# Kernel tuning notes

Hardware: AMD Instinct MI355X
Metric: run time of the kernel (lower is better)

## Reference

```python
import jax, jax.numpy as jnp
import numpy as np

NUM_ITERS = 3

def squash(t, axis):
    # scale = |t|^2/(1+|t|^2); out = scale * t / |t|
    sn = jnp.sum(t * t, axis=axis, keepdims=True)
    return (sn / (1.0 + sn)) * t / jnp.sqrt(sn)


def setup_inputs() -> dict:
    key = jax.random.key(0)
    k1, k2, k3, k4 = jax.random.split(key, 4)
    B = 128
    inputs = jax.random.normal(k1, (B, 256, 20, 20), dtype=jnp.float32)
    conv_w = jax.random.normal(k2, (8, 32, 256, 9, 9), dtype=jnp.float32) * 0.05
    conv_b = jax.random.normal(k3, (8, 32), dtype=jnp.float32) * 0.05
    route_weights = jax.random.normal(k4, (10, 1152, 8, 16), dtype=jnp.float32)
    return {"inputs": inputs, "conv_w": conv_w, "conv_b": conv_b,
            "route_weights": route_weights}


def reference(inputs, conv_w, conv_b, route_weights):
    B = inputs.shape[0]
    K, O, Cin, kh, kw = conv_w.shape          # 8 capsules, 32 out-chans each
    # --- primary capsules: 8 parallel convs fused into one grouped-output conv ---
    w = conv_w.reshape(K * O, Cin, kh, kw)
    out = jax.lax.conv_general_dilated(
        inputs, w, window_strides=(2, 2), padding='VALID',
        dimension_numbers=('NCHW', 'OIHW', 'NCHW'))  # [B, K*O, 6, 6]
    out = out + conv_b.reshape(K * O)[None, :, None, None]
    H = out.shape[-1]
    x = out.reshape(B, K, O * H * H).transpose(0, 2, 1)  # [B, 1152, 8]
    x = squash(x, axis=2)
    # --- routing layer ---
    # prediction_vectors: x[None,:,:,None,:] @ W[:,None,:,:,:] -> [10,B,1152,1,16]
    pred = jnp.einsum('bri,crio->cbro', x, route_weights)[:, :, :, None, :]
    logits = jnp.zeros_like(pred)
    v = None
    for i in range(NUM_ITERS):
        # routing_softmax(dim=2): softmax over the routes axis (faithful to source)
        c = jax.nn.softmax(logits, axis=2)
        s = jnp.sum(c * pred, axis=2, keepdims=True)  # [10,B,1,1,16]
        v = squash(s, axis=1)                          # squash default dim=1 (batch) -- faithful
        if i != NUM_ITERS - 1:
            logits = logits + jnp.sum(pred * v, axis=-1, keepdims=True)
    # [10,B,1,1,16] -> squeeze -> [10,B,16] -> permute(1,0,2) -> [B,10,16]
    return jnp.squeeze(v).transpose(1, 0, 2)
```

## Files before the change

kernel.cpp:

```cpp
#include <hip/hip_runtime.h>
#include <math.h>

typedef _Float16 f16;
typedef _Float16 f16x8 __attribute__((ext_vector_type(8)));
typedef float f32x4 __attribute__((ext_vector_type(4)));
typedef float f32x8 __attribute__((ext_vector_type(8)));

#define AS1 __attribute__((address_space(1)))
#define AS3 __attribute__((address_space(3)))

__device__ __forceinline__ void gld_lds16(const f16* g, f16* l) {
#if defined(__has_builtin) && __has_builtin(__builtin_amdgcn_global_load_lds)
    __builtin_amdgcn_global_load_lds((const AS1 void*)g, (AS3 void*)l, 16, 0, 0);
#else
    *(uint4*)l = *(const uint4*)g;
#endif
}

__global__ __launch_bounds__(256) void transpose_input(
    const float* __restrict__ inp, f16* __restrict__ out)
{
    const int b = blockIdx.x, c0 = blockIdx.y * 32, p0 = blockIdx.z * 32;
    const int tx = threadIdx.x, ty = threadIdx.y;
    __shared__ float t[32][33];
#pragma unroll
    for (int j = 0; j < 4; ++j) {
        int c = ty + j * 8, p = p0 + tx;
        if (p < 400) t[c][tx] = inp[((size_t)b * 256 + c0 + c) * 400 + p];
    }
    __syncthreads();
#pragma unroll
    for (int j = 0; j < 4; ++j) {
        int p = p0 + ty + j * 8;
        if (p < 400) out[((size_t)b * 400 + p) * 256 + c0 + tx] = (f16)t[tx][ty + j * 8];
    }
}

__global__ __launch_bounds__(256) void permute_w(
    const float* __restrict__ cw, f16* __restrict__ w_t)
{
    const int n = blockIdx.x, t = threadIdx.x;
    __shared__ f16 buf[81 * 258];
    const float* src = cw + (size_t)n * 20736;
    for (int i = t; i < 20736; i += 256) {
        int cin = i / 81, p = i - cin * 81;
        buf[p * 258 + cin] = (f16)src[i];
    }
    __syncthreads();
    f16* dst = w_t + (size_t)n * 20736;
    for (int j = t; j < 20736; j += 256) {
        int p = j >> 8, cin = j & 255;
        dst[j] = buf[p * 258 + cin];
    }
}

#define SPLITK 9
#define CITER 72
__global__ __launch_bounds__(256) void conv_mfma(
    const f16* __restrict__ in_t,
    const f16* __restrict__ w_t,
    float* __restrict__ part)
{
    __shared__ f16 As[2][128 * 32];
    __shared__ f16 Bs[2][128 * 32];
    const int tid = threadIdx.x;
    const int lane = tid & 63, wave = tid >> 6;
    const int wm = wave >> 1, wn = wave & 1;
    const int m0 = blockIdx.x * 128, n0 = blockIdx.y * 128;
    const int kz = blockIdx.z;

    int srcA[2], srcB[2];
#pragma unroll
    for (int i = 0; i < 2; ++i) {
        int pairp = i * 32 + (tid >> 3);
        int chunk8 = (tid & 7) ^ (pairp & 7);
        int e = chunk8 >> 2, q4 = chunk8 & 3;
        int m = m0 + pairp * 2 + e;
        int b = m / 36, hw = m - b * 36;
        int ho = hw / 6, wo = hw - ho * 6;
        srcA[i] = ((b * 20 + 2 * ho) * 20 + 2 * wo) * 256 + q4 * 8;
        int n = n0 + pairp * 2 + e;
        srcB[i] = n * 20736 + q4 * 8;
    }

    f32x4 acc[4][4] = {};
    const int row = lane & 15, quad = lane >> 4;
    const int kc_base = kz * CITER;

    {
        int kc = kc_base;
        int p = kc >> 3, cq = kc & 7;
        int kh = p / 9, kw = p - kh * 9;
        int koffA = (kh * 20 + kw) * 256 + cq * 32;
        int koffB = kc * 32;
#pragma unroll
        for (int i = 0; i < 2; ++i) {
            gld_lds16(in_t + srcA[i] + koffA, &As[0][i * 2048 + tid * 8]);
            gld_lds16(w_t + srcB[i] + koffB, &Bs[0][i * 2048 + tid * 8]);
        }
    }

    for (int it = 0; it < CITER; ++it) {
        const int cur = it & 1;
        __syncthreads();
        if (it + 1 < CITER) {
            int kc = kc_base + it + 1;
            int p = kc >> 3, cq = kc & 7;
            int kh = p / 9, kw = p - kh * 9;
            int koffA = (kh * 20 + kw) * 256 + cq * 32;
            int koffB = kc * 32;
#pragma unroll
            for (int i = 0; i < 2; ++i) {
                gld_lds16(in_t + srcA[i] + koffA, &As[cur ^ 1][i * 2048 + tid * 8]);
                gld_lds16(w_t + srcB[i] + koffB, &Bs[cur ^ 1][i * 2048 + tid * 8]);
            }
        }
        f16x8 af[4], bf[4];
#pragma unroll
        for (int mt = 0; mt < 4; ++mt) {
            int m = wm * 64 + mt * 16 + row;
            int ph8 = (((m & 1) << 2) + quad) ^ ((m >> 1) & 7);
            af[mt] = *(const f16x8*)(&As[cur][(m >> 1) * 64 + ph8 * 8]);
        }
#pragma unroll
        for (int nt = 0; nt < 4; ++nt) {
            int n = wn * 64 + nt * 16 + row;
            int ph8 = (((n & 1) << 2) + quad) ^ ((n >> 1) & 7);
            bf[nt] = *(const f16x8*)(&Bs[cur][(n >> 1) * 64 + ph8 * 8]);
        }
#pragma unroll
        for (int mt = 0; mt < 4; ++mt)
#pragma unroll
            for (int nt = 0; nt < 4; ++nt)
                acc[mt][nt] = __builtin_amdgcn_mfma_f32_16x16x32_f16(
                    af[mt], bf[nt], acc[mt][nt], 0, 0, 0);
    }

    const int col = lane & 15, qr = (lane >> 4) * 4;
    float* pb = part + (size_t)kz * 4608 * 256;
#pragma unroll
    for (int mt = 0; mt < 4; ++mt)
#pragma unroll
        for (int rg = 0; rg < 4; ++rg) {
            int m = m0 + wm * 64 + mt * 16 + qr + rg;
#pragma unroll
            for (int nt = 0; nt < 4; ++nt) {
                int n = n0 + wn * 64 + nt * 16 + col;
                pb[(size_t)m * 256 + n] = acc[mt][nt][rg];
            }
        }
}

__global__ __launch_bounds__(256) void combine_squash(
    const float* __restrict__ part, const float* __restrict__ bias,
    float* __restrict__ x)
{
    int idx = blockIdx.x * 256 + threadIdx.x;
    int m = idx >> 5, o = idx & 31;
    int b = m / 36, hw = m - b * 36;
    float val[8];
#pragma unroll
    for (int k = 0; k < 8; ++k) val[k] = bias[k * 32 + o];
#pragma unroll
    for (int s = 0; s < SPLITK; ++s) {
        const float* p = part + ((size_t)s * 4608 + m) * 256 + o;
#pragma unroll
        for (int k = 0; k < 8; ++k) val[k] += p[k * 32];
    }
    float sn = 0.f;
#pragma unroll
    for (int k = 0; k < 8; ++k) sn += val[k] * val[k];
    float scale = sqrtf(sn) / (1.f + sn);
    int r = o * 36 + hw;
    float* xp = x + ((size_t)b * 1152 + r) * 8;
#pragma unroll
    for (int k = 0; k < 8; ++k) xp[k] = val[k] * scale;
}

__global__ __launch_bounds__(256) void pred_kernel(
    const float* __restrict__ x, const float* __restrict__ rw,
    f16* __restrict__ pred)
{
    const int c = blockIdx.x, r0 = blockIdx.y * 32, b0 = blockIdx.z * 32;
    const int tid = threadIdx.x;
    const int o = tid & 15, rp = tid >> 4;
    const int r = r0 + rp * 2;

    float W0[8], W1[8];
    const float* wb = rw + ((size_t)(c * 1152 + r) * 8) * 16 + o;
#pragma unroll
    for (int k = 0; k < 8; ++k) { W0[k] = wb[k * 16]; W1[k] = wb[128 + k * 16]; }

    for (int b = b0; b < b0 + 32; ++b) {
        const float4* xp = (const float4*)(x + ((size_t)b * 1152 + r) * 8);
        float4 xa = xp[0], xb = xp[1], xc = xp[2], xd = xp[3];
        float p0 = xa.x * W0[0] + xa.y * W0[1] + xa.z * W0[2] + xa.w * W0[3]
                 + xb.x * W0[4] + xb.y * W0[5] + xb.z * W0[6] + xb.w * W0[7];
        float p1 = xc.x * W1[0] + xc.y * W1[1] + xc.z * W1[2] + xc.w * W1[3]
                 + xd.x * W1[4] + xd.y * W1[5] + xd.z * W1[6] + xd.w * W1[7];
        f16* pb = pred + ((size_t)(c * 128 + b) * 1152 + r) * 16 + o;
        pb[0]  = (f16)p0;
        pb[16] = (f16)p1;
    }
}

__global__ __launch_bounds__(256) void route_f16(
    const f16* __restrict__ pred, const float* __restrict__ s_in,
    const float* __restrict__ z_in, const float* __restrict__ a_in,
    float* __restrict__ a_out, float* __restrict__ s_out, float* __restrict__ z_out)
{
    const int c = blockIdx.x, b = blockIdx.y, tid = threadIdx.x;
    const size_t base = (size_t)(c * 128 + b) * 1152;

    __shared__ float vs[16];
    __shared__ float mat[128][17];
    __shared__ float red[256][16];
    __shared__ float red2[16][16];
    __shared__ float zred[256];
    __shared__ float zpart[16];

    if (s_in) {
        if (tid < 128) {
            float zin = z_in ? 1.f / z_in[c * 128 + tid] : (1.f / 1152.f);
            const float* sp = s_in + (size_t)(c * 128 + tid) * 16;
#pragma unroll
            for (int o = 0; o < 16; ++o) mat[tid][o] = sp[o] * zin;
        }
        __syncthreads();
        if (tid < 16) {
            float sn = 0.f;
            for (int i = 0; i < 128; ++i) { float q = mat[i][tid]; sn += q * q; }
            vs[tid] = mat[b][tid] * sqrtf(sn) / (1.f + sn);
        }
        __syncthreads();
    }

    float sacc[16];
#pragma unroll
    for (int o = 0; o < 16; ++o) sacc[o] = 0.f;
    float zacc = 0.f;

    for (int r = tid; r < 1152; r += 256) {
        const f16x8* pp = (const f16x8*)(pred + (base + r) * 16);
        f32x8 q0 = __builtin_convertvector(pp[0], f32x8);
        f32x8 q1 = __builtin_convertvector(pp[1], f32x8);
        float e;
        if (s_in) {
            float contrib = 0.f;
#pragma unroll
            for (int j = 0; j < 8; ++j) contrib += q0[j] * vs[j] + q1[j] * vs[j + 8];
            float an = contrib + (a_in ? a_in[base + r] : 0.f);
            if (a_out) a_out[base + r] = an;
            e = __expf(an);
        } else {
            e = 1.f;
        }
#pragma unroll
        for (int j = 0; j < 8; ++j) { sacc[j] += e * q0[j]; sacc[j + 8] += e * q1[j]; }
        zacc += e;
    }

#pragma unroll
    for (int o = 0; o < 16; ++o) red[tid][o] = sacc[o];
    zred[tid] = zacc;
    __syncthreads();
    {
        const int o = tid & 15, seg = tid >> 4;
        float t = 0.f;
#pragma unroll
        for (int j = 0; j < 16; ++j) t += red[seg * 16 + j][o];
        red2[seg][o] = t;
        if (tid < 16) {
            float tz = 0.f;
#pragma unroll
            for (int j = 0; j < 16; ++j) tz += zred[tid * 16 + j];
            zpart[tid] = tz;
        }
    }
    __syncthreads();
    if (tid < 16) {
        float t = 0.f;
#pragma unroll
        for (int seg = 0; seg < 16; ++seg) t += red2[seg][tid];
        s_out[(size_t)(c * 128 + b) * 16 + tid] = t;
    } else if (tid == 16) {
        float tz = 0.f;
#pragma unroll
        for (int j = 0; j < 16; ++j) tz += zpart[j];
        z_out[c * 128 + b] = tz;
    }
}

__global__ __launch_bounds__(128) void squash_final(
    const float* __restrict__ s, const float* __restrict__ z,
    float* __restrict__ out)
{
    const int c = blockIdx.x, b = threadIdx.x;
    float sv[16];
    const float* sp = s + ((size_t)c * 128 + b) * 16;
    float zin = 1.f / z[c * 128 + b];
#pragma unroll
    for (int o = 0; o < 16; ++o) sv[o] = sp[o] * zin;
    __shared__ float m[16][129];
#pragma unroll
    for (int o = 0; o < 16; ++o) m[o][b] = sv[o] * sv[o];
    __syncthreads();
    __shared__ float sn[16];
    if (b < 16) {
        float t = 0.f;
        for (int i = 0; i < 128; ++i) t += m[b][i];
        sn[b] = t;
    }
    __syncthreads();
#pragma unroll
    for (int o = 0; o < 16; ++o) {
        float scale = sqrtf(sn[o]) / (1.f + sn[o]);
        out[((size_t)b * 10 + c) * 16 + o] = sv[o] * scale;
    }
}

extern "C" void kernel_launch(void* const* d_in, const int* in_sizes, int n_in,
                              void* d_out, int out_size, void* d_ws, size_t ws_size,
                              hipStream_t stream)
{
    (void)in_sizes; (void)n_in; (void)out_size; (void)ws_size;
    const float* inp = (const float*)d_in[0];
    const float* cw  = (const float*)d_in[1];
    const float* cb  = (const float*)d_in[2];
    const float* rw  = (const float*)d_in[3];
    float* out = (float*)d_out;

    char* ws = (char*)d_ws;
    float* part = (float*)(ws);
    f16*   in_t = (f16*)(ws + 42467328);
    f16*   w_t  = (f16*)(ws + 68681728);
    float* x    = (float*)(ws + 79298560);
    float* a    = (float*)(ws + 84017152);
    float* sA   = (float*)(ws + 89915392);
    float* zA   = (float*)(ws + 89997312);
    float* sB   = (float*)(ws + 90002432);
    float* zB   = (float*)(ws + 90084352);
    f16*   pred = (f16*)(ws);

    transpose_input<<<dim3(128, 8, 13), dim3(32, 8), 0, stream>>>(inp, in_t);
    permute_w<<<256, 256, 0, stream>>>(cw, w_t);
    conv_mfma<<<dim3(36, 2, SPLITK), 256, 0, stream>>>(in_t, w_t, part);
    combine_squash<<<576, 256, 0, stream>>>(part, cb, x);
    pred_kernel<<<dim3(10, 36, 4), 256, 0, stream>>>(x, rw, pred);

    route_f16<<<dim3(10, 128), 256, 0, stream>>>(pred, nullptr, nullptr, nullptr,
                                                 nullptr, sA, zA);
    route_f16<<<dim3(10, 128), 256, 0, stream>>>(pred, sA, zA, nullptr,
                                                 a, sB, zB);
    route_f16<<<dim3(10, 128), 256, 0, stream>>>(pred, sB, zB, a,
                                                 nullptr, sA, zA);
    squash_final<<<10, 128, 0, stream>>>(sA, zA, out);
}
```

Measured before the change: 287.4 us.

## Fuse first routing sum into pred kernel, fp16 split-K partials with doubled split

The first routing iteration, which uses uniform coupling, is folded into the prediction kernel. Per-batch sums are accumulated through wave shuffles, shared-memory atomics and then global atomics into a zeroed buffer, so one full pass over pred is dropped. The conv split-K factor is doubled and its partials are stored in fp16 to halve the partial-sum traffic, and the workspace layout is rearranged to fit. The costs are fp16 rounding of partials, added atomic contention, and non-deterministic summation order.

```diff
diff --git a/kernel.cpp b/kernel.cpp
--- a/kernel.cpp
+++ b/kernel.cpp
@@ -54,12 +54,12 @@
     }
 }
 
-#define SPLITK 9
-#define CITER 72
+#define SPLITK 18
+#define CITER 36
 __global__ __launch_bounds__(256) void conv_mfma(
     const f16* __restrict__ in_t,
     const f16* __restrict__ w_t,
-    float* __restrict__ part)
+    f16* __restrict__ part)
 {
     __shared__ f16 As[2][128 * 32];
     __shared__ f16 Bs[2][128 * 32];
@@ -137,7 +137,7 @@
     }
 
     const int col = lane & 15, qr = (lane >> 4) * 4;
-    float* pb = part + (size_t)kz * 4608 * 256;
+    f16* pb = part + (size_t)kz * 4608 * 256;
 #pragma unroll
     for (int mt = 0; mt < 4; ++mt)
 #pragma unroll
@@ -146,13 +146,13 @@
 #pragma unroll
             for (int nt = 0; nt < 4; ++nt) {
                 int n = n0 + wn * 64 + nt * 16 + col;
-                pb[(size_t)m * 256 + n] = acc[mt][nt][rg];
+                pb[(size_t)m * 256 + n] = (f16)acc[mt][nt][rg];
             }
         }
 }
 
 __global__ __launch_bounds__(256) void combine_squash(
-    const float* __restrict__ part, const float* __restrict__ bias,
+    const f16* __restrict__ part, const float* __restrict__ bias,
     float* __restrict__ x)
 {
     int idx = blockIdx.x * 256 + threadIdx.x;
@@ -163,9 +163,9 @@
     for (int k = 0; k < 8; ++k) val[k] = bias[k * 32 + o];
 #pragma unroll
     for (int s = 0; s < SPLITK; ++s) {
-        const float* p = part + ((size_t)s * 4608 + m) * 256 + o;
-#pragma unroll
-        for (int k = 0; k < 8; ++k) val[k] += p[k * 32];
+        const f16* p = part + ((size_t)s * 4608 + m) * 256 + o;
+#pragma unroll
+        for (int k = 0; k < 8; ++k) val[k] += (float)p[k * 32];
     }
     float sn = 0.f;
 #pragma unroll
@@ -177,21 +177,26 @@
     for (int k = 0; k < 8; ++k) xp[k] = val[k] * scale;
 }
 
-__global__ __launch_bounds__(256) void pred_kernel(
+__global__ __launch_bounds__(256) void pred_s0(
     const float* __restrict__ x, const float* __restrict__ rw,
-    f16* __restrict__ pred)
+    f16* __restrict__ pred, float* __restrict__ s0)
 {
     const int c = blockIdx.x, r0 = blockIdx.y * 32, b0 = blockIdx.z * 32;
     const int tid = threadIdx.x;
     const int o = tid & 15, rp = tid >> 4;
     const int r = r0 + rp * 2;
 
+    __shared__ float s_sh[32 * 16];
+    s_sh[tid] = 0.f; s_sh[tid + 256] = 0.f;
+
     float W0[8], W1[8];
     const float* wb = rw + ((size_t)(c * 1152 + r) * 8) * 16 + o;
 #pragma unroll
     for (int k = 0; k < 8; ++k) { W0[k] = wb[k * 16]; W1[k] = wb[128 + k * 16]; }
-
-    for (int b = b0; b < b0 + 32; ++b) {
+    __syncthreads();
+
+    for (int bb = 0; bb < 32; ++bb) {
+        const int b = b0 + bb;
         const float4* xp = (const float4*)(x + ((size_t)b * 1152 + r) * 8);
         float4 xa = xp[0], xb = xp[1], xc = xp[2], xd = xp[3];
         float p0 = xa.x * W0[0] + xa.y * W0[1] + xa.z * W0[2] + xa.w * W0[3]
@@ -201,6 +206,15 @@
         f16* pb = pred + ((size_t)(c * 128 + b) * 1152 + r) * 16 + o;
         pb[0]  = (f16)p0;
         pb[16] = (f16)p1;
+        float ps = p0 + p1;
+        ps += __shfl_xor(ps, 16);
+        ps += __shfl_xor(ps, 32);
+        if ((tid & 63) < 16) atomicAdd(&s_sh[bb * 16 + o], ps);
+    }
+    __syncthreads();
+    for (int i = tid; i < 512; i += 256) {
+        int bb = i >> 4, oo = i & 15;
+        atomicAdd(&s0[((size_t)c * 128 + b0 + bb) * 16 + oo], s_sh[i]);
     }
 }
 
@@ -219,7 +233,7 @@
     __shared__ float zred[256];
     __shared__ float zpart[16];
 
-    if (s_in) {
+    {
         if (tid < 128) {
             float zin = z_in ? 1.f / z_in[c * 128 + tid] : (1.f / 1152.f);
             const float* sp = s_in + (size_t)(c * 128 + tid) * 16;
@@ -244,17 +258,12 @@
         const f16x8* pp = (const f16x8*)(pred + (base + r) * 16);
         f32x8 q0 = __builtin_convertvector(pp[0], f32x8);
         f32x8 q1 = __builtin_convertvector(pp[1], f32x8);
-        float e;
-        if (s_in) {
-            float contrib = 0.f;
-#pragma unroll
-            for (int j = 0; j < 8; ++j) contrib += q0[j] * vs[j] + q1[j] * vs[j + 8];
-            float an = contrib + (a_in ? a_in[base + r] : 0.f);
-            if (a_out) a_out[base + r] = an;
-            e = __expf(an);
-        } else {
-            e = 1.f;
-        }
+        float contrib = 0.f;
+#pragma unroll
+        for (int j = 0; j < 8; ++j) contrib += q0[j] * vs[j] + q1[j] * vs[j + 8];
+        float an = contrib + (a_in ? a_in[base + r] : 0.f);
+        if (a_out) a_out[base + r] = an;
+        float e = __expf(an);
 #pragma unroll
         for (int j = 0; j < 8; ++j) { sacc[j] += e * q0[j]; sacc[j + 8] += e * q1[j]; }
         zacc += e;
@@ -331,26 +340,26 @@
     float* out = (float*)d_out;
 
     char* ws = (char*)d_ws;
-    float* part = (float*)(ws);
-    f16*   in_t = (f16*)(ws + 42467328);
-    f16*   w_t  = (f16*)(ws + 68681728);
-    float* x    = (float*)(ws + 79298560);
-    float* a    = (float*)(ws + 84017152);
-    float* sA   = (float*)(ws + 89915392);
-    float* zA   = (float*)(ws + 89997312);
-    float* sB   = (float*)(ws + 90002432);
-    float* zB   = (float*)(ws + 90084352);
+    f16*   part = (f16*)(ws);
     f16*   pred = (f16*)(ws);
+    float* x    = (float*)(ws + 47185920);
+    float* a    = (float*)(ws + 51904512);
+    float* sA   = (float*)(ws + 57802752);
+    float* zA   = (float*)(ws + 57884672);
+    float* sB   = (float*)(ws + 57889792);
+    float* zB   = (float*)(ws + 57971712);
+    f16*   in_t = (f16*)(ws + 57976832);
+    f16*   w_t  = (f16*)(ws + 84191232);
 
     transpose_input<<<dim3(128, 8, 13), dim3(32, 8), 0, stream>>>(inp, in_t);
     permute_w<<<256, 256, 0, stream>>>(cw, w_t);
     conv_mfma<<<dim3(36, 2, SPLITK), 256, 0, stream>>>(in_t, w_t, part);
     combine_squash<<<576, 256, 0, stream>>>(part, cb, x);
-    pred_kernel<<<dim3(10, 36, 4), 256, 0, stream>>>(x, rw, pred);
-
-    route_f16<<<dim3(10, 128), 256, 0, stream>>>(pred, nullptr, nullptr, nullptr,
-                                                 nullptr, sA, zA);
-    route_f16<<<dim3(10, 128), 256, 0, stream>>>(pred, sA, zA, nullptr,
+
+    hipMemsetAsync(sA, 0, 81920, stream);
+    pred_s0<<<dim3(10, 36, 4), 256, 0, stream>>>(x, rw, pred, sA);
+
+    route_f16<<<dim3(10, 128), 256, 0, stream>>>(pred, sA, nullptr, nullptr,
                                                  a, sB, zB);
     route_f16<<<dim3(10, 128), 256, 0, stream>>>(pred, sB, zB, a,
                                                  nullptr, sA, zA);
```

Result: faster. 280.5 us (-2.4%).
